# Performance work log

Hardware: AMD Instinct MI355X
Metric: run time of the kernel (lower is better)

Reference implementation:

```python
import jax, jax.numpy as jnp
import numpy as np
import math

B, N, C, H = 64, 197, 768, 12
D = C // H
MLP = 4 * C
TOKEN_KEEP = 0.7
ATTN_KEEP = 0.7
LN_EPS = 1e-5
ATTN_EPS = 1e-6
NUM_KEEP = math.ceil((N - 1) * TOKEN_KEEP)           # 138 kept patch tokens
NUM_KEEP_ATTN = math.ceil(NUM_KEEP * ATTN_KEEP)      # kept attention entries per row


def setup_inputs() -> dict:
    key = jax.random.key(0)
    ks = jax.random.split(key, 12)
    s = 0.02
    return {
        "x": jax.random.normal(ks[0], (B, N, C), jnp.float32),
        "attn_mask": jnp.ones((B, N, N), jnp.float32),
        "norm1_g": jnp.ones((C,), jnp.float32),
        "norm1_b": jnp.zeros((C,), jnp.float32),
        "qkv_w": jax.random.normal(ks[1], (C, 3 * C), jnp.float32) * s,
        "qkv_b": jnp.zeros((3 * C,), jnp.float32),
        "proj_w": jax.random.normal(ks[2], (C, C), jnp.float32) * s,
        "proj_b": jnp.zeros((C,), jnp.float32),
        "norm2_g": jnp.ones((C,), jnp.float32),
        "norm2_b": jnp.zeros((C,), jnp.float32),
        "fc1_w": jax.random.normal(ks[3], (C, MLP), jnp.float32) * s,
        "fc1_b": jnp.zeros((MLP,), jnp.float32),
        "fc2_w": jax.random.normal(ks[4], (MLP, C), jnp.float32) * s,
        "fc2_b": jnp.zeros((C,), jnp.float32),
    }


def _layernorm(x, g, b):
    mu = jnp.mean(x, axis=-1, keepdims=True)
    var = jnp.mean(jnp.square(x - mu), axis=-1, keepdims=True)
    return (x - mu) * jax.lax.rsqrt(var + LN_EPS) * g + b


def reference(x, attn_mask, norm1_g, norm1_b, qkv_w, qkv_b, proj_w, proj_b,
              norm2_g, norm2_b, fc1_w, fc1_b, fc2_w, fc2_b):
    scale = D ** (-0.5)
    h = _layernorm(x, norm1_g, norm1_b)
    qkv = (h @ qkv_w + qkv_b).reshape(B, N, 3, H, D).transpose(2, 0, 3, 1, 4)
    q, k, v = qkv[0], qkv[1], qkv[2]                       # [B,H,N,D]

    scores = jnp.einsum("bhnd,bhmd->bhnm", q, k) * scale   # [B,H,N,N]
    scores = scores - jnp.max(scores, axis=-1, keepdims=True)
    attn = jnp.exp(scores.astype(jnp.float32)) * attn_mask[:, None].astype(jnp.float32)
    attn = (attn + ATTN_EPS / N) / (jnp.sum(attn, axis=-1, keepdims=True) + ATTN_EPS)

    x_att = jnp.einsum("bhnm,bhmd->bhnd", attn, v).transpose(0, 2, 1, 3).reshape(B, N, C)
    x_att = x_att @ proj_w + proj_b

    cls_attn = jnp.sum(attn[:, :, 0, 1:], axis=1) / H      # [B, N-1]
    patch_attn = jnp.sum(attn[:, :, 1:, 1:], axis=1) / H   # [B, N-1, N-1]

    x = x + x_att

    # token pruning: keep top NUM_KEEP patches by cls attention
    _, token_idx = jax.lax.top_k(cls_attn, NUM_KEEP)       # [B, NUM_KEEP]
    x_patches = jnp.take_along_axis(x[:, 1:], token_idx[:, :, None], axis=1)
    x = jnp.concatenate([x[:, 0:1], x_patches], axis=1)    # [B, NUM_KEEP+1, C]

    # attention pruning: binary mask from topk of pruned patch attention
    pp = jnp.take_along_axis(patch_attn, token_idx[:, :, None], axis=1)
    pp = jnp.take_along_axis(pp, token_idx[:, None, :], axis=2)   # [B, rN, rN]
    top_val, _ = jax.lax.top_k(pp, NUM_KEEP_ATTN)
    mask_p = (pp >= top_val[:, :, -1:]).astype(jnp.float32)
    new_mask = jnp.ones((B, NUM_KEEP + 1, NUM_KEEP + 1), jnp.float32)
    new_mask = new_mask.at[:, 1:, 1:].set(mask_p)

    h2 = _layernorm(x, norm2_g, norm2_b)
    mlp = jax.nn.gelu(h2 @ fc1_w + fc1_b, approximate=False) @ fc2_w + fc2_b
    x = x + mlp
    return x, token_idx, new_mask, cls_attn
```

## Files before the change

### kernel.cpp

```cpp
#include <hip/hip_runtime.h>
#include <hip/hip_bf16.h>
#include <math.h>

#define BB 64
#define NN 197
#define CC 768
#define HH 12
#define MLPD 3072
#define NKEEP 138
#define NKEEPA 97
#define NPATCH 196
#define NOUT_TOK 139
#define STILE 32

typedef __attribute__((ext_vector_type(8))) short bf16x8;
typedef __attribute__((ext_vector_type(4))) float f32x4;

static __device__ inline ushort f2bf(float f) {
    __hip_bfloat16 h = __float2bfloat16(f);
    return *(ushort*)&h;
}
static __device__ inline float bf2f(ushort u) {
    __hip_bfloat16 h;
    *(ushort*)&h = u;
    return __bfloat162float(h);
}

__device__ inline double exp64(double x) {
    const double L2E    = 1.4426950408889634074;
    const double LN2_HI = 6.93147180369123816490e-01;
    const double LN2_LO = 1.90821492927058770002e-10;
    double nf = rint(x * L2E);
    double r  = fma(-nf, LN2_HI, x);
    r = fma(-nf, LN2_LO, r);
    double p = 1.0 / 3628800.0;
    p = fma(p, r, 1.0 / 362880.0);
    p = fma(p, r, 1.0 / 40320.0);
    p = fma(p, r, 1.0 / 5040.0);
    p = fma(p, r, 1.0 / 720.0);
    p = fma(p, r, 1.0 / 120.0);
    p = fma(p, r, 1.0 / 24.0);
    p = fma(p, r, 1.0 / 6.0);
    p = fma(p, r, 0.5);
    p = fma(p, r, 1.0);
    p = fma(p, r, 1.0);
    long long bits = ((long long)(1023 + (int)nf)) << 52;
    return p * __longlong_as_double(bits);
}

__device__ inline double wave_max64(double v) {
#pragma unroll
    for (int o = 32; o; o >>= 1) v = fmax(v, __shfl_xor(v, o));
    return v;
}
__device__ inline double wave_sum64(double v) {
#pragma unroll
    for (int o = 32; o; o >>= 1) v += __shfl_xor(v, o);
    return v;
}

__device__ inline int gat_src(int row, const int* __restrict__ tok) {
    if (row > BB * NOUT_TOK - 1) row = BB * NOUT_TOK - 1;
    const int b = row / NOUT_TOK, i = row % NOUT_TOK;
    return b * NN + ((i == 0) ? 0 : (1 + tok[b * NKEEP + i - 1]));
}

__global__ __launch_bounds__(256) void ln_kernel(const float* __restrict__ in,
                                                 const float* __restrict__ g,
                                                 const float* __restrict__ b,
                                                 float* __restrict__ out32,
                                                 ushort* __restrict__ out16) {
    const int row = blockIdx.x;
    const int t = threadIdx.x;
    const int lane = t & 63, w = t >> 6;
    const float* xr = in + (size_t)row * CC;
    __shared__ double wred[4];

    const float v0 = xr[t], v1 = xr[t + 256], v2 = xr[t + 512];
    double s = (double)v0 + (double)v1 + (double)v2;
    s = wave_sum64(s);
    if (lane == 0) wred[w] = s;
    __syncthreads();
    const double mu = (wred[0] + wred[1] + wred[2] + wred[3]) * (1.0 / CC);

    const double d0 = (double)v0 - mu, d1 = (double)v1 - mu, d2 = (double)v2 - mu;
    double vs = d0 * d0 + d1 * d1 + d2 * d2;
    vs = wave_sum64(vs);
    __syncthreads();
    if (lane == 0) wred[w] = vs;
    __syncthreads();
    const double inv = 1.0 / sqrt((wred[0] + wred[1] + wred[2] + wred[3]) * (1.0 / CC) + 1e-5);

    const int cs[3] = {t, t + 256, t + 512};
    const double dv[3] = {d0, d1, d2};
#pragma unroll
    for (int i = 0; i < 3; i++) {
        float v = (float)(dv[i] * inv * (double)g[cs[i]] + (double)b[cs[i]]);
        if (out32) out32[(size_t)row * CC + cs[i]] = v;
        if (out16) out16[(size_t)row * CC + cs[i]] = f2bf(v);
    }
}

__global__ __launch_bounds__(256) void gemm_qk_kernel(const float* __restrict__ A,
                                                      const float* __restrict__ Bw,
                                                      const float* __restrict__ bias,
                                                      float* __restrict__ C,
                                                      int K, int ldb, int ldc) {
    __shared__ float As[32][132];
    __shared__ float Bs[32][68];
    const int tid = threadIdx.x;
    const int tx = tid & 15;
    const int ty = tid >> 4;
    const int m0 = blockIdx.y * 128;
    const int n0 = blockIdx.x * 64;

    const int a_k = tid & 31, a_g = tid >> 5;
    const int b_n = tid & 63, b_kg = tid >> 6;

    float acc[8][4];
    double dacc[8][4];
#pragma unroll
    for (int i = 0; i < 8; i++)
#pragma unroll
        for (int j = 0; j < 4; j++) { acc[i][j] = 0.f; dacc[i][j] = 0.0; }

    float a_reg[16], b_reg[8];
#pragma unroll
    for (int i = 0; i < 16; i++)
        a_reg[i] = A[(size_t)(m0 + a_g * 16 + i) * 768 + a_k];
#pragma unroll
    for (int i = 0; i < 8; i++)
        b_reg[i] = Bw[(size_t)(b_kg * 8 + i) * ldb + n0 + b_n];

    for (int k0 = 0; k0 < K; k0 += 32) {
        __syncthreads();
#pragma unroll
        for (int i = 0; i < 4; i++)
            *(float4*)&As[a_k][a_g * 16 + i * 4] =
                make_float4(a_reg[i * 4], a_reg[i * 4 + 1], a_reg[i * 4 + 2], a_reg[i * 4 + 3]);
#pragma unroll
        for (int i = 0; i < 8; i++) Bs[b_kg * 8 + i][b_n] = b_reg[i];
        __syncthreads();
        if (k0 + 32 < K) {
#pragma unroll
            for (int i = 0; i < 16; i++)
                a_reg[i] = A[(size_t)(m0 + a_g * 16 + i) * 768 + k0 + 32 + a_k];
#pragma unroll
            for (int i = 0; i < 8; i++)
                b_reg[i] = Bw[(size_t)(k0 + 32 + b_kg * 8 + i) * ldb + n0 + b_n];
        }
#pragma unroll
        for (int k = 0; k < 32; k++) {
            float4 a0 = *(const float4*)&As[k][ty * 8];
            float4 a1 = *(const float4*)&As[k][ty * 8 + 4];
            float4 bv = *(const float4*)&Bs[k][tx * 4];
            float a_[8] = {a0.x, a0.y, a0.z, a0.w, a1.x, a1.y, a1.z, a1.w};
            float b_[4] = {bv.x, bv.y, bv.z, bv.w};
#pragma unroll
            for (int i = 0; i < 8; i++)
#pragma unroll
                for (int j = 0; j < 4; j++)
                    acc[i][j] = fmaf(a_[i], b_[j], acc[i][j]);
            if ((k & 15) == 15) {
#pragma unroll
                for (int i = 0; i < 8; i++)
#pragma unroll
                    for (int j = 0; j < 4; j++) { dacc[i][j] += (double)acc[i][j]; acc[i][j] = 0.f; }
            }
        }
    }

#pragma unroll
    for (int i = 0; i < 8; i++) {
        const int row = m0 + ty * 8 + i;
#pragma unroll
        for (int j = 0; j < 4; j++) {
            const int col = n0 + tx * 4 + j;
            C[(size_t)row * ldc + col] = (float)(dacc[i][j] + (double)bias[col]);
        }
    }
}

template <int MODE, bool OUT_BF16, bool GATHER>
__global__ __launch_bounds__(512) void mfma_gemm(const ushort* __restrict__ A,
                                                 const ushort* __restrict__ Bt,
                                                 const float* __restrict__ bias,
                                                 const float* __restrict__ res,
                                                 void* __restrict__ Cout,
                                                 const int* __restrict__ tok,
                                                 int M, int K, int Nc) {
    __shared__ ushort As[128][40];
    __shared__ ushort Bs[128][40];
    const int tid = threadIdx.x;
    const int w = tid >> 6, lane = tid & 63;
    const int m0 = blockIdx.y * 128, n0 = blockIdx.x * 128;
    const int wr = w >> 2, wc = w & 3;
    const int sr = tid >> 2, sk = (tid & 3) * 8;
    const int lr = lane & 15, lq = lane >> 4;
    const int kq = lq * 8;

    size_t arow = m0 + sr;
    if (GATHER) arow = gat_src(m0 + sr, tok);

    f32x4 acc[4][2];
#pragma unroll
    for (int i = 0; i < 4; i++)
#pragma unroll
        for (int j = 0; j < 2; j++) acc[i][j] = (f32x4){0.f, 0.f, 0.f, 0.f};

    bf16x8 a_pre = *(const bf16x8*)&A[arow * K + sk];
    bf16x8 b_pre = *(const bf16x8*)&Bt[(size_t)(n0 + sr) * K + sk];

    for (int k0 = 0; k0 < K; k0 += 32) {
        __syncthreads();
        *(bf16x8*)&As[sr][sk] = a_pre;
        *(bf16x8*)&Bs[sr][sk] = b_pre;
        __syncthreads();
        if (k0 + 32 < K) {
            a_pre = *(const bf16x8*)&A[arow * K + k0 + 32 + sk];
            b_pre = *(const bf16x8*)&Bt[(size_t)(n0 + sr) * K + k0 + 32 + sk];
        }

        bf16x8 af[4], bfr[2];
#pragma unroll
        for (int i = 0; i < 4; i++) af[i] = *(const bf16x8*)&As[wr * 64 + i * 16 + lr][kq];
#pragma unroll
        for (int j = 0; j < 2; j++) bfr[j] = *(const bf16x8*)&Bs[wc * 32 + j * 16 + lr][kq];
#pragma unroll
        for (int i = 0; i < 4; i++)
#pragma unroll
            for (int j = 0; j < 2; j++)
                acc[i][j] = __builtin_amdgcn_mfma_f32_16x16x32_bf16(af[i], bfr[j], acc[i][j], 0, 0, 0);
    }

#pragma unroll
    for (int i = 0; i < 4; i++)
#pragma unroll
        for (int r = 0; r < 4; r++) {
            const int row = m0 + wr * 64 + i * 16 + lq * 4 + r;
            if (row >= M) continue;
            size_t rrow = row;
            if (GATHER && MODE == 1) rrow = gat_src(row, tok);
#pragma unroll
            for (int j = 0; j < 2; j++) {
#pragma unroll
                for (int e = 0; e < 4; e++) {
                    const int col = n0 + wc * 32 + j * 16 + lr;
                    (void)e;
                }
            }
#pragma unroll
            for (int j = 0; j < 2; j++) {
                const int col = n0 + wc * 32 + j * 16 + lr;
                float v = acc[i][j][r] + bias[col];
                if (MODE == 1) v += res[rrow * Nc + col];
                if (MODE == 2) v = 0.5f * v * (1.0f + erff(v * 0.70710678118654752f));
                if (OUT_BF16) ((ushort*)Cout)[(size_t)row * Nc + col] = f2bf(v);
                else ((float*)Cout)[(size_t)row * Nc + col] = v;
            }
        }
}

__global__ __launch_bounds__(256) void transw_kernel(const float* __restrict__ W, int ldw,
                                                     ushort* __restrict__ Wt, int K) {
    __shared__ float tile[32][33];
    const int n0 = blockIdx.x * 32, k0 = blockIdx.y * 32;
    const int tx = threadIdx.x & 31, ty = threadIdx.x >> 5;
#pragma unroll
    for (int r = 0; r < 32; r += 8)
        tile[ty + r][tx] = W[(size_t)(k0 + ty + r) * ldw + n0 + tx];
    __syncthreads();
#pragma unroll
    for (int r = 0; r < 32; r += 8)
        Wt[(size_t)(n0 + ty + r) * K + k0 + tx] = f2bf(tile[tx][ty + r]);
}

__global__ __launch_bounds__(256) void transv_kernel(const ushort* __restrict__ vbf,
                                                     ushort* __restrict__ vbfT) {
    __shared__ ushort tile[32][72];
    const int mt = blockIdx.x, hh = blockIdx.y, b = blockIdx.z;
    const int t = threadIdx.x;
    {
        const int mm = t >> 3, dq = (t & 7) * 8;
        const int m = mt * 32 + mm;
        bf16x8 v = (bf16x8){0, 0, 0, 0, 0, 0, 0, 0};
        if (m < NN)
            v = *(const bf16x8*)&vbf[((size_t)(b * NN + m)) * CC + hh * 64 + dq];
        *(bf16x8*)&tile[mm][dq] = v;
    }
    __syncthreads();
    {
        const int d = t >> 2, mq = (t & 3) * 8;
        ushort tmp[8];
#pragma unroll
        for (int j = 0; j < 8; j++) tmp[j] = tile[mq + j][d];
        *(bf16x8*)&vbfT[(((size_t)(b * HH + hh)) * 64 + d) * 224 + mt * 32 + mq] =
            *(bf16x8*)tmp;
    }
}

#define KSTR 68
#define PSTR 232
__global__ __launch_bounds__(512) void attn_kernel(const float* __restrict__ qk,
                                                   const ushort* __restrict__ vbfT,
                                                   const float* __restrict__ amask,
                                                   ushort* __restrict__ xatt_bf,
                                                   double* __restrict__ cls64,
                                                   double* __restrict__ patch64) {
    const int tile = blockIdx.x;
    const int b = blockIdx.y;
    const int row0 = tile * STILE;
    const int nrows = min(STILE, NN - row0);
    const int t = threadIdx.x;
    const int w = t >> 6, lane = t & 63;

    __shared__ __align__(16) char pool[61776];
    float*  Kf = (float*)pool;
    float*  Qf = (float*)(pool + 53584);
    ushort* Vt = (ushort*)pool;
    ushort* Pb = (ushort*)(pool + 32768);

    int mcol[4], mc[4];
    bool mok[4];
#pragma unroll
    for (int c = 0; c < 4; c++) {
        mcol[c] = lane + 64 * c;
        mok[c] = mcol[c] < NN;
        mc[c] = mok[c] ? mcol[c] : 0;
    }
    int rloc[4];
    bool rok[4];
#pragma unroll
    for (int rr = 0; rr < 4; rr++) {
        rloc[rr] = w + 8 * rr;
        rok[rr] = rloc[rr] < nrows;
    }

    float mv[4][4];
#pragma unroll
    for (int rr = 0; rr < 4; rr++)
#pragma unroll
        for (int c = 0; c < 4; c++)
            mv[rr][c] = (rok[rr] && mok[c])
                ? amask[((size_t)(b * NN + row0 + rloc[rr])) * NN + mcol[c]] : 0.f;

    const int rt = w >> 2, ct = w & 3;
    const int lr = lane & 15, lq = lane >> 4;

    double hacc[4][4] = {};

    for (int h = 0; h < HH; ++h) {
        __syncthreads();
        for (int idx = t; idx < NN * 16; idx += 512) {
            int m = idx >> 4, dq = (idx & 15) * 4;
            *(float4*)&Kf[m * KSTR + dq] =
                *(const float4*)&qk[((size_t)(b * NN + m)) * 1536 + 768 + h * 64 + dq];
        }
        for (int idx = t; idx < nrows * 64; idx += 512) {
            int r = idx >> 6, d = idx & 63;
            Qf[r * 64 + d] = qk[((size_t)(b * NN + row0 + r)) * 1536 + h * 64 + d];
        }
        __syncthreads();

        double s[4][4] = {};
        {
            float facc[4][4] = {};
            for (int d0 = 0; d0 < 64; d0 += 4) {
                float4 qv[4];
#pragma unroll
                for (int rr = 0; rr < 4; rr++)
                    qv[rr] = rok[rr] ? *(const float4*)&Qf[rloc[rr] * 64 + d0]
                                     : make_float4(0.f, 0.f, 0.f, 0.f);
#pragma unroll
                for (int c = 0; c < 4; c++) {
                    float4 kv = *(const float4*)&Kf[mc[c] * KSTR + d0];
#pragma unroll
                    for (int rr = 0; rr < 4; rr++) {
                        facc[rr][c] = fmaf(qv[rr].x, kv.x,
                                      fmaf(qv[rr].y, kv.y,
                                      fmaf(qv[rr].z, kv.z,
                                      fmaf(qv[rr].w, kv.w, facc[rr][c]))));
                    }
                }
                if ((d0 & 4) == 4) {
#pragma unroll
                    for (int rr = 0; rr < 4; rr++)
#pragma unroll
                        for (int c = 0; c < 4; c++) {
                            s[rr][c] += (double)facc[rr][c];
                            facc[rr][c] = 0.f;
                        }
                }
            }
        }
        __syncthreads();

#pragma unroll
        for (int rr = 0; rr < 4; rr++) {
            if (!rok[rr]) continue;
            double sc[4];
#pragma unroll
            for (int c = 0; c < 4; c++)
                sc[c] = mok[c] ? s[rr][c] * 0.125 : -1.0e300;
            double mx = fmax(fmax(sc[0], sc[1]), fmax(sc[2], sc[3]));
            mx = wave_max64(mx);
            double e[4];
#pragma unroll
            for (int c = 0; c < 4; c++)
                e[c] = mok[c] ? exp64(sc[c] - mx) * (double)mv[rr][c] : 0.0;
            double S = wave_sum64(e[0] + e[1] + e[2] + e[3]);
            double inv = 1.0 / (S + 1e-6);
            const double epsn = 1e-6 / 197.0;
#pragma unroll
            for (int c = 0; c < 4; c++) {
                if (!mok[c]) continue;
                double pr = (e[c] + epsn) * inv;
                Pb[rloc[rr] * PSTR + mcol[c]] = f2bf((float)pr);
                hacc[rr][c] += pr;
            }
        }
        for (int idx = t; idx < 32 * 27; idx += 512) {
            int r = idx / 27, m = 197 + idx % 27;
            Pb[r * PSTR + m] = 0;
        }
        for (int idx = t; idx < (STILE - nrows) * 197; idx += 512) {
            int r = nrows + idx / 197, m = idx % 197;
            Pb[r * PSTR + m] = 0;
        }
        {
            const ushort* vsrc = vbfT + ((size_t)(b * HH + h)) * 64 * 224;
            for (int idx = t; idx < 64 * 28; idx += 512) {
                int d = idx / 28, mb = (idx % 28) * 8;
                *(bf16x8*)&Vt[d * PSTR + mb] = *(const bf16x8*)&vsrc[d * 224 + mb];
            }
        }
        __syncthreads();

        f32x4 acc = (f32x4){0.f, 0.f, 0.f, 0.f};
#pragma unroll
        for (int k0 = 0; k0 < 224; k0 += 32) {
            bf16x8 pa = *(const bf16x8*)&Pb[(rt * 16 + lr) * PSTR + k0 + lq * 8];
            bf16x8 vb = *(const bf16x8*)&Vt[(ct * 16 + lr) * PSTR + k0 + lq * 8];
            acc = __builtin_amdgcn_mfma_f32_16x16x32_bf16(pa, vb, acc, 0, 0, 0);
        }
#pragma unroll
        for (int rg = 0; rg < 4; rg++) {
            const int row = rt * 16 + lq * 4 + rg;
            if (row < nrows)
                xatt_bf[((size_t)(b * NN + row0 + row)) * CC + h * 64 + ct * 16 + lr] =
                    f2bf(acc[rg]);
        }
    }

#pragma unroll
    for (int rr = 0; rr < 4; rr++) {
        if (!rok[rr]) continue;
        const int grow = row0 + rloc[rr];
#pragma unroll
        for (int c = 0; c < 4; c++) {
            if (!mok[c] || mcol[c] < 1) continue;
            double v = hacc[rr][c] * (1.0 / 12.0);
            if (grow == 0)
                cls64[(size_t)b * NPATCH + mcol[c] - 1] = v;
            else
                patch64[((size_t)b * NPATCH + grow - 1) * NPATCH + (mcol[c] - 1)] = v;
        }
    }
}

__global__ __launch_bounds__(256) void topk_kernel(const double* __restrict__ cls,
                                                   int* __restrict__ tok,
                                                   float* __restrict__ tok_f,
                                                   float* __restrict__ out_cls) {
    const int b = blockIdx.x;
    const int t = threadIdx.x;
    __shared__ double v[NPATCH];
    if (t < NPATCH) {
        v[t] = cls[(size_t)b * NPATCH + t];
        out_cls[(size_t)b * NPATCH + t] = (float)v[t];
    }
    __syncthreads();
    if (t < NPATCH) {
        const double mvv = v[t];
        int cnt = 0;
        for (int i = 0; i < NPATCH; ++i) {
            double vi = v[i];
            cnt += (vi > mvv) || (vi == mvv && i < t);
        }
        if (cnt < NKEEP) {
            tok[b * NKEEP + cnt] = t;
            tok_f[b * NKEEP + cnt] = (float)t;
        }
    }
}

__global__ __launch_bounds__(256) void mask_kernel(const double* __restrict__ patch,
                                                   const int* __restrict__ tok,
                                                   float* __restrict__ omask) {
    const int i = blockIdx.x;
    const int b = blockIdx.y;
    const int t = threadIdx.x;
    float* orow = omask + ((size_t)b * NOUT_TOK + i) * NOUT_TOK;
    if (i == 0) {
        if (t < NOUT_TOK) orow[t] = 1.f;
        return;
    }
    __shared__ int tj[NKEEP];
    __shared__ double pr[NKEEP];
    if (t < NKEEP) tj[t] = tok[b * NKEEP + t];
    __syncthreads();
    const int ti = tj[i - 1];
    if (t < NKEEP) pr[t] = patch[((size_t)b * NPATCH + ti) * NPATCH + tj[t]];
    __syncthreads();
    if (t == 255) orow[0] = 1.f;
    if (t < NKEEP) {
        const double val = pr[t];
        int cnt = 0;
        for (int l = 0; l < NKEEP; ++l) cnt += (pr[l] > val);
        orow[1 + t] = (cnt < NKEEPA) ? 1.f : 0.f;
    }
}

extern "C" void kernel_launch(void* const* d_in, const int* in_sizes, int n_in,
                              void* d_out, int out_size, void* d_ws, size_t ws_size,
                              hipStream_t stream) {
    const float* x      = (const float*)d_in[0];
    const float* amask  = (const float*)d_in[1];
    const float* n1g    = (const float*)d_in[2];
    const float* n1b    = (const float*)d_in[3];
    const float* qkv_w  = (const float*)d_in[4];
    const float* qkv_b  = (const float*)d_in[5];
    const float* proj_w = (const float*)d_in[6];
    const float* proj_b = (const float*)d_in[7];
    const float* n2g    = (const float*)d_in[8];
    const float* n2b    = (const float*)d_in[9];
    const float* fc1_w  = (const float*)d_in[10];
    const float* fc1_b  = (const float*)d_in[11];
    const float* fc2_w  = (const float*)d_in[12];
    const float* fc2_b  = (const float*)d_in[13];

    float* ws = (float*)d_ws;
    const size_t A_OFF = 0;
    const size_t C_OFF = 9682944;
    const size_t B_OFF = 14524416;
    const size_t D_OFF = 33890304;
    const size_t E_OFF = 38731776;
    const size_t F_OFF = 43573248;
    const size_t G_OFF = 48490496;
    const size_t H_OFF = 48515584;
    const size_t I_OFF = 48524416;

    float*  h        = ws + A_OFF;
    ushort* v_bfT    = (ushort*)(ws + A_OFF);
    ushort* mlp_bf   = (ushort*)(ws + A_OFF);
    ushort* h_bf     = (ushort*)(ws + C_OFF);
    float*  qk       = ws + B_OFF;
    float*  xp       = ws + B_OFF;
    ushort* h2_bf    = (ushort*)(ws + B_OFF + 10248192);
    ushort* v_bf     = (ushort*)(ws + D_OFF);
    ushort* xatt_bf  = (ushort*)(ws + E_OFF);
    double* patch64  = (double*)(ws + F_OFF);
    ushort* fc1_t    = (ushort*)(ws + F_OFF);
    ushort* fc2_t    = (ushort*)(ws + F_OFF + 1179648);
    double* cls64    = (double*)(ws + G_OFF);
    int*    tok      = (int*)(ws + H_OFF);
    ushort* wv_t     = (ushort*)(ws + I_OFF);
    ushort* proj_t   = (ushort*)(ws + I_OFF + 294912);

    float* out_x   = (float*)d_out;
    float* out_idx = out_x + 6832128;
    float* out_msk = out_idx + 8832;
    float* out_cls = out_msk + 1236544;

    const int ROWS1 = BB * NN;
    const int ROWS2 = BB * NOUT_TOK;

    ln_kernel<<<ROWS1, 256, 0, stream>>>(x, n1g, n1b, h, h_bf);
    transw_kernel<<<dim3(24, 24), 256, 0, stream>>>(qkv_w + 1536, 2304, wv_t, 768);
    transw_kernel<<<dim3(24, 24), 256, 0, stream>>>(proj_w, 768, proj_t, 768);
    gemm_qk_kernel<<<dim3(1536 / 64, 12672 / 128), 256, 0, stream>>>(
        h, qkv_w, qkv_b, qk, 768, 2304, 1536);
    mfma_gemm<0, true, false><<<dim3(768 / 128, 12672 / 128), 512, 0, stream>>>(
        h_bf, wv_t, qkv_b + 1536, nullptr, v_bf, nullptr, ROWS1, 768, 768);
    transv_kernel<<<dim3(7, HH, BB), 256, 0, stream>>>(v_bf, v_bfT);
    attn_kernel<<<dim3(7, BB), 512, 0, stream>>>(qk, v_bfT, amask, xatt_bf, cls64, patch64);
    topk_kernel<<<BB, 256, 0, stream>>>(cls64, tok, out_idx, out_cls);
    mfma_gemm<1, false, true><<<dim3(768 / 128, 8960 / 128), 512, 0, stream>>>(
        xatt_bf, proj_t, proj_b, x, xp, tok, ROWS2, 768, 768);
    mask_kernel<<<dim3(NOUT_TOK, BB), 256, 0, stream>>>(patch64, tok, out_msk);
    transw_kernel<<<dim3(96, 24), 256, 0, stream>>>(fc1_w, 3072, fc1_t, 768);
    transw_kernel<<<dim3(24, 96), 256, 0, stream>>>(fc2_w, 768, fc2_t, 3072);
    ln_kernel<<<ROWS2, 256, 0, stream>>>(xp, n2g, n2b, nullptr, h2_bf);
    mfma_gemm<2, true, false><<<dim3(3072 / 128, 8960 / 128), 512, 0, stream>>>(
        h2_bf, fc1_t, fc1_b, nullptr, mlp_bf, nullptr, ROWS2, 768, 3072);
    mfma_gemm<1, false, false><<<dim3(768 / 128, 8960 / 128), 512, 0, stream>>>(
        mlp_bf, fc2_t, fc2_b, xp, out_x, nullptr, ROWS2, 3072, 768);
}
```

Baseline: 1.185 ms.

## Fuse QK fp32 GEMM and V bf16 MFMA GEMM into one interleaved launch

Merges the FP32 Q/K projection GEMM and the bf16 MFMA V projection GEMM into a single kernel. Block IDs are interleaved so two QK tiles and one V tile alternate across the grid, with the V path now using 64x128 tiles on 256 threads. This removes one launch and lets the compute-heavy fp32 FMA blocks and the MFMA blocks share the device concurrently. The cost is a larger register and shared-memory footprint per block, set by the heavier QK path, which may lower occupancy. A dead loop is also removed from the generic GEMM epilogue.

```diff
diff --git a/kernel.cpp b/kernel.cpp
--- a/kernel.cpp
+++ b/kernel.cpp
@@ -101,83 +101,151 @@
     }
 }
 
-__global__ __launch_bounds__(256) void gemm_qk_kernel(const float* __restrict__ A,
-                                                      const float* __restrict__ Bw,
-                                                      const float* __restrict__ bias,
-                                                      float* __restrict__ C,
-                                                      int K, int ldb, int ldc) {
-    __shared__ float As[32][132];
-    __shared__ float Bs[32][68];
+__global__ __launch_bounds__(256) void qkv_mega_kernel(
+    const float* __restrict__ A, const float* __restrict__ Bw,
+    const float* __restrict__ bias, float* __restrict__ C,
+    const ushort* __restrict__ Abf, const ushort* __restrict__ Bt,
+    const float* __restrict__ vbias, ushort* __restrict__ Vout) {
+    __shared__ __align__(16) char pool[25600];
+    const int bid = blockIdx.x;
     const int tid = threadIdx.x;
-    const int tx = tid & 15;
-    const int ty = tid >> 4;
-    const int m0 = blockIdx.y * 128;
-    const int n0 = blockIdx.x * 64;
-
-    const int a_k = tid & 31, a_g = tid >> 5;
-    const int b_n = tid & 63, b_kg = tid >> 6;
-
-    float acc[8][4];
-    double dacc[8][4];
-#pragma unroll
-    for (int i = 0; i < 8; i++)
-#pragma unroll
-        for (int j = 0; j < 4; j++) { acc[i][j] = 0.f; dacc[i][j] = 0.0; }
-
-    float a_reg[16], b_reg[8];
-#pragma unroll
-    for (int i = 0; i < 16; i++)
-        a_reg[i] = A[(size_t)(m0 + a_g * 16 + i) * 768 + a_k];
-#pragma unroll
-    for (int i = 0; i < 8; i++)
-        b_reg[i] = Bw[(size_t)(b_kg * 8 + i) * ldb + n0 + b_n];
-
-    for (int k0 = 0; k0 < K; k0 += 32) {
-        __syncthreads();
-#pragma unroll
-        for (int i = 0; i < 4; i++)
-            *(float4*)&As[a_k][a_g * 16 + i * 4] =
-                make_float4(a_reg[i * 4], a_reg[i * 4 + 1], a_reg[i * 4 + 2], a_reg[i * 4 + 3]);
-#pragma unroll
-        for (int i = 0; i < 8; i++) Bs[b_kg * 8 + i][b_n] = b_reg[i];
-        __syncthreads();
-        if (k0 + 32 < K) {
-#pragma unroll
-            for (int i = 0; i < 16; i++)
-                a_reg[i] = A[(size_t)(m0 + a_g * 16 + i) * 768 + k0 + 32 + a_k];
-#pragma unroll
-            for (int i = 0; i < 8; i++)
-                b_reg[i] = Bw[(size_t)(k0 + 32 + b_kg * 8 + i) * ldb + n0 + b_n];
-        }
-#pragma unroll
-        for (int k = 0; k < 32; k++) {
-            float4 a0 = *(const float4*)&As[k][ty * 8];
-            float4 a1 = *(const float4*)&As[k][ty * 8 + 4];
-            float4 bv = *(const float4*)&Bs[k][tx * 4];
-            float a_[8] = {a0.x, a0.y, a0.z, a0.w, a1.x, a1.y, a1.z, a1.w};
-            float b_[4] = {bv.x, bv.y, bv.z, bv.w};
-#pragma unroll
-            for (int i = 0; i < 8; i++)
+
+    bool is_v;
+    int qk_idx = 0, v_idx = 0;
+    if (bid < 3546) {
+        const int r = bid % 3;
+        is_v = (r == 2);
+        if (is_v) v_idx = bid / 3;
+        else      qk_idx = (bid / 3) * 2 + r;
+    } else {
+        is_v = false;
+        qk_idx = 2364 + (bid - 3546);
+    }
+
+    if (!is_v) {
+        float* As = (float*)pool;
+        float* Bs = (float*)(pool + 16896);
+        const int tx = tid & 15;
+        const int ty = tid >> 4;
+        const int m0 = (qk_idx / 24) * 128;
+        const int n0 = (qk_idx % 24) * 64;
+        const int K = 768, ldb = 2304, ldc = 1536;
+
+        const int a_k = tid & 31, a_g = tid >> 5;
+        const int b_n = tid & 63, b_kg = tid >> 6;
+
+        float acc[8][4];
+        double dacc[8][4];
+#pragma unroll
+        for (int i = 0; i < 8; i++)
+#pragma unroll
+            for (int j = 0; j < 4; j++) { acc[i][j] = 0.f; dacc[i][j] = 0.0; }
+
+        float a_reg[16], b_reg[8];
+#pragma unroll
+        for (int i = 0; i < 16; i++)
+            a_reg[i] = A[(size_t)(m0 + a_g * 16 + i) * 768 + a_k];
+#pragma unroll
+        for (int i = 0; i < 8; i++)
+            b_reg[i] = Bw[(size_t)(b_kg * 8 + i) * ldb + n0 + b_n];
+
+        for (int k0 = 0; k0 < K; k0 += 32) {
+            __syncthreads();
+#pragma unroll
+            for (int i = 0; i < 4; i++)
+                *(float4*)&As[a_k * 132 + a_g * 16 + i * 4] =
+                    make_float4(a_reg[i * 4], a_reg[i * 4 + 1], a_reg[i * 4 + 2], a_reg[i * 4 + 3]);
+#pragma unroll
+            for (int i = 0; i < 8; i++) Bs[(b_kg * 8 + i) * 68 + b_n] = b_reg[i];
+            __syncthreads();
+            if (k0 + 32 < K) {
+#pragma unroll
+                for (int i = 0; i < 16; i++)
+                    a_reg[i] = A[(size_t)(m0 + a_g * 16 + i) * 768 + k0 + 32 + a_k];
+#pragma unroll
+                for (int i = 0; i < 8; i++)
+                    b_reg[i] = Bw[(size_t)(k0 + 32 + b_kg * 8 + i) * ldb + n0 + b_n];
+            }
+#pragma unroll
+            for (int k = 0; k < 32; k++) {
+                float4 a0 = *(const float4*)&As[k * 132 + ty * 8];
+                float4 a1 = *(const float4*)&As[k * 132 + ty * 8 + 4];
+                float4 bv = *(const float4*)&Bs[k * 68 + tx * 4];
+                float a_[8] = {a0.x, a0.y, a0.z, a0.w, a1.x, a1.y, a1.z, a1.w};
+                float b_[4] = {bv.x, bv.y, bv.z, bv.w};
+#pragma unroll
+                for (int i = 0; i < 8; i++)
+#pragma unroll
+                    for (int j = 0; j < 4; j++)
+                        acc[i][j] = fmaf(a_[i], b_[j], acc[i][j]);
+                if ((k & 15) == 15) {
+#pragma unroll
+                    for (int i = 0; i < 8; i++)
+#pragma unroll
+                        for (int j = 0; j < 4; j++) { dacc[i][j] += (double)acc[i][j]; acc[i][j] = 0.f; }
+                }
+            }
+        }
+
+#pragma unroll
+        for (int i = 0; i < 8; i++) {
+            const int row = m0 + ty * 8 + i;
+            if (row >= BB * NN) continue;
+#pragma unroll
+            for (int j = 0; j < 4; j++) {
+                const int col = n0 + tx * 4 + j;
+                C[(size_t)row * ldc + col] = (float)(dacc[i][j] + (double)bias[col]);
+            }
+        }
+    } else {
+        ushort* vAs = (ushort*)pool;
+        ushort* vBs = (ushort*)(pool + 5120);
+        const int w = tid >> 6, lane = tid & 63;
+        const int m0 = (v_idx / 6) * 64, n0 = (v_idx % 6) * 128;
+        const int wm = (w >> 1) * 32, wn = (w & 1) * 64;
+        const int K = 768;
+
+        f32x4 acc[2][4];
+#pragma unroll
+        for (int i = 0; i < 2; i++)
+#pragma unroll
+            for (int j = 0; j < 4; j++) acc[i][j] = (f32x4){0.f, 0.f, 0.f, 0.f};
+
+        const int ar = tid >> 2, ak = (tid & 3) * 8;
+        const int bc = tid >> 1, bk = (tid & 1) * 16;
+        const int lr = lane & 15, lq = lane >> 4;
+        const int kq = lq * 8;
+
+        for (int k0 = 0; k0 < K; k0 += 32) {
+            __syncthreads();
+            *(bf16x8*)&vAs[ar * 40 + ak] = *(const bf16x8*)&Abf[(size_t)(m0 + ar) * K + k0 + ak];
+            *(bf16x8*)&vBs[bc * 40 + bk] = *(const bf16x8*)&Bt[(size_t)(n0 + bc) * K + k0 + bk];
+            *(bf16x8*)&vBs[bc * 40 + bk + 8] = *(const bf16x8*)&Bt[(size_t)(n0 + bc) * K + k0 + bk + 8];
+            __syncthreads();
+
+            bf16x8 af[2], bfr[4];
+#pragma unroll
+            for (int i = 0; i < 2; i++) af[i] = *(const bf16x8*)&vAs[(wm + i * 16 + lr) * 40 + kq];
+#pragma unroll
+            for (int j = 0; j < 4; j++) bfr[j] = *(const bf16x8*)&vBs[(wn + j * 16 + lr) * 40 + kq];
+#pragma unroll
+            for (int i = 0; i < 2; i++)
 #pragma unroll
                 for (int j = 0; j < 4; j++)
-                    acc[i][j] = fmaf(a_[i], b_[j], acc[i][j]);
-            if ((k & 15) == 15) {
-#pragma unroll
-                for (int i = 0; i < 8; i++)
-#pragma unroll
-                    for (int j = 0; j < 4; j++) { dacc[i][j] += (double)acc[i][j]; acc[i][j] = 0.f; }
-            }
-        }
-    }
-
-#pragma unroll
-    for (int i = 0; i < 8; i++) {
-        const int row = m0 + ty * 8 + i;
-#pragma unroll
-        for (int j = 0; j < 4; j++) {
-            const int col = n0 + tx * 4 + j;
-            C[(size_t)row * ldc + col] = (float)(dacc[i][j] + (double)bias[col]);
-        }
+                    acc[i][j] = __builtin_amdgcn_mfma_f32_16x16x32_bf16(af[i], bfr[j], acc[i][j], 0, 0, 0);
+        }
+
+#pragma unroll
+        for (int i = 0; i < 2; i++)
+#pragma unroll
+            for (int j = 0; j < 4; j++)
+#pragma unroll
+                for (int r = 0; r < 4; r++) {
+                    const int row = m0 + wm + i * 16 + lq * 4 + r;
+                    const int col = n0 + wn + j * 16 + lr;
+                    float v = acc[i][j][r] + vbias[col];
+                    Vout[(size_t)row * 768 + col] = f2bf(v);
+                }
     }
 }
 
@@ -243,14 +311,6 @@
             if (GATHER && MODE == 1) rrow = gat_src(row, tok);
 #pragma unroll
             for (int j = 0; j < 2; j++) {
-#pragma unroll
-                for (int e = 0; e < 4; e++) {
-                    const int col = n0 + wc * 32 + j * 16 + lr;
-                    (void)e;
-                }
-            }
-#pragma unroll
-            for (int j = 0; j < 2; j++) {
                 const int col = n0 + wc * 32 + j * 16 + lr;
                 float v = acc[i][j][r] + bias[col];
                 if (MODE == 1) v += res[rrow * Nc + col];
@@ -578,10 +638,8 @@
     ln_kernel<<<ROWS1, 256, 0, stream>>>(x, n1g, n1b, h, h_bf);
     transw_kernel<<<dim3(24, 24), 256, 0, stream>>>(qkv_w + 1536, 2304, wv_t, 768);
     transw_kernel<<<dim3(24, 24), 256, 0, stream>>>(proj_w, 768, proj_t, 768);
-    gemm_qk_kernel<<<dim3(1536 / 64, 12672 / 128), 256, 0, stream>>>(
-        h, qkv_w, qkv_b, qk, 768, 2304, 1536);
-    mfma_gemm<0, true, false><<<dim3(768 / 128, 12672 / 128), 512, 0, stream>>>(
-        h_bf, wv_t, qkv_b + 1536, nullptr, v_bf, nullptr, ROWS1, 768, 768);
+    qkv_mega_kernel<<<3558, 256, 0, stream>>>(h, qkv_w, qkv_b, qk,
+                                              h_bf, wv_t, qkv_b + 1536, v_bf);
     transv_kernel<<<dim3(7, HH, BB), 256, 0, stream>>>(v_bf, v_bfT);
     attn_kernel<<<dim3(7, BB), 512, 0, stream>>>(qk, v_bfT, amask, xatt_bf, cls64, patch64);
     topk_kernel<<<BB, 256, 0, stream>>>(cls64, tok, out_idx, out_cls);
```

Result: slower. 1.381 ms (+16.5%).
